# Kernel optimization log

Measured on AMD Instinct MI355X. Metric: run time of the kernel, lower is better.

The kernel has to match this reference:

```python
import jax, jax.numpy as jnp
import numpy as np

N_NODES = 50000
N_EDGES = 800000
N_FEAT = 512
N_HEADS = 8
OUT_PER_HEAD = 32  # nhid // nheads = 256 // 8
ALPHA = 0.2  # LeakyReLU negative slope


def setup_inputs() -> dict:
    key = jax.random.key(0)
    ks = jax.random.split(key, 7)
    h = jax.random.normal(ks[0], (N_NODES, N_FEAT), dtype=jnp.float32)
    src = jax.random.randint(ks[1], (N_EDGES,), 0, N_NODES)
    dst = jax.random.randint(ks[2], (N_EDGES,), 0, N_NODES)
    # per-head linear W: [H, F, O], bias [H, O]; attention vector a: [H, 2O], bias [H]
    W = jax.random.normal(ks[3], (N_HEADS, N_FEAT, OUT_PER_HEAD), dtype=jnp.float32) * 0.05
    Wb = jax.random.normal(ks[4], (N_HEADS, OUT_PER_HEAD), dtype=jnp.float32) * 0.05
    a = jax.random.normal(ks[5], (N_HEADS, 2 * OUT_PER_HEAD), dtype=jnp.float32) * 0.05
    ab = jax.random.normal(ks[6], (N_HEADS,), dtype=jnp.float32) * 0.05
    return {"h": h, "src": src, "dst": dst, "W": W, "Wb": Wb, "a": a, "ab": ab}


def reference(h, src, dst, W, Wb, a, ab):
    N = h.shape[0]
    H, F_in, O = W.shape
    # Per-head projection Wh = W(h): [N, H, O]
    Wh = jnp.einsum('nf,hfo->nho', h, W) + Wb
    # a @ concat(Wh_src, Wh_dst) == a_src @ Wh_src + a_dst @ Wh_dst
    a_src, a_dst = a[:, :O], a[:, O:]
    e_s = jnp.einsum('nho,ho->nh', Wh, a_src)  # [N, H]
    e_d = jnp.einsum('nho,ho->nh', Wh, a_dst)
    e = e_s[src] + e_d[dst] + ab               # [E, H]
    e = jnp.where(e > 0, e, ALPHA * e)         # LeakyReLU
    # Segment softmax over incoming edges of each destination node
    m = jax.ops.segment_max(e, dst, num_segments=N)        # [N, H]
    m = jnp.where(jnp.isfinite(m), m, jnp.zeros_like(m))   # isolated nodes
    w = jnp.exp(e - m[dst])                                # [E, H]
    denom = jax.ops.segment_sum(w, dst, num_segments=N)    # [N, H]
    att = w / jnp.where(denom[dst] > 0, denom[dst], 1.0)   # [E, H]
    # Weighted aggregation of source projections, per head, then concat heads
    out = jax.ops.segment_sum(att[:, :, None] * Wh[src], dst, num_segments=N)  # [N, H, O]
    return out.reshape(N, H * O)
```

## Files before the change

### kernel.cpp

```cpp
#include <hip/hip_runtime.h>
#include <math.h>

#define ALPHA 0.2f

constexpr int F_IN  = 512;
constexpr int HO    = 256;
constexpr int NHEAD = 8;

using bf16x8 = __attribute__((ext_vector_type(8))) short;
using bf16x4 = __attribute__((ext_vector_type(4))) short;
using f32x4  = __attribute__((ext_vector_type(4))) float;

__device__ __forceinline__ ushort f2bf(float f) {
    uint u = __float_as_uint(f);
    uint r = (u + 0x7FFFu + ((u >> 16) & 1u)) >> 16;
    return (ushort)r;
}
__device__ __forceinline__ float bf2f(ushort b) {
    return __uint_as_float(((uint)b) << 16);
}

__global__ __launch_bounds__(256) void prep_kernel(const float* __restrict__ W,
                                                   ushort* __restrict__ Wf,
                                                   const int* __restrict__ dst,
                                                   int* __restrict__ cnt,
                                                   int* __restrict__ rnk, int E) {
    const int bid = blockIdx.x;
    const int t = threadIdx.x;
    if (bid < 64) {
        int g = bid * 256 + t;
        int l   = g & 63;
        int oct = (g >> 6) & 15;
        int ks  = g >> 10;
        int oc  = oct * 16 + (l & 15);
        int hh  = oc >> 5, oo = oc & 31;
        int kb  = ks * 32 + (l >> 4) * 8;
        ushort v[8];
#pragma unroll
        for (int j = 0; j < 8; ++j)
            v[j] = f2bf(W[((size_t)hh * F_IN + kb + j) * 32 + oo]);
        bf16x8 o = { (short)v[0], (short)v[1], (short)v[2], (short)v[3],
                     (short)v[4], (short)v[5], (short)v[6], (short)v[7] };
        *(bf16x8*)(Wf + (size_t)g * 8) = o;
    } else {
        int base = (bid - 64) * 1024;
#pragma unroll
        for (int q = 0; q < 4; ++q) {
            int i = base + q * 256 + t;
            if (i < E) rnk[i] = atomicAdd(&cnt[dst[i]], 1);
        }
    }
}

__global__ __launch_bounds__(256) void scan1_kernel(const int* __restrict__ cnt,
                                                    int* __restrict__ bsum, int N) {
    __shared__ int red[256];
    const int t = threadIdx.x;
    const int b0 = blockIdx.x * 1024;
    int s = 0;
#pragma unroll
    for (int q = 0; q < 4; ++q) {
        int i = b0 + t * 4 + q;
        if (i < N) s += cnt[i];
    }
    red[t] = s;
    __syncthreads();
    for (int st = 128; st > 0; st >>= 1) {
        if (t < st) red[t] += red[t + st];
        __syncthreads();
    }
    if (t == 0) bsum[blockIdx.x] = red[0];
}

__global__ __launch_bounds__(64) void scan2_kernel(int* __restrict__ bsum, int nblk) {
    int l = threadIdx.x;
    int x = (l < nblk) ? bsum[l] : 0;
    int inc = x;
    for (int d = 1; d < 64; d <<= 1) {
        int v = __shfl_up(inc, d);
        if (l >= d) inc += v;
    }
    if (l < nblk) bsum[l] = inc - x;
}

__global__ __launch_bounds__(256) void scan3_kernel(const int* __restrict__ cnt,
                                                    const int* __restrict__ bsum,
                                                    int* __restrict__ off, int N, int E) {
    __shared__ int part[256];
    const int t = threadIdx.x;
    const int b0 = blockIdx.x * 1024;
    int v[4];
    int s = 0;
#pragma unroll
    for (int q = 0; q < 4; ++q) {
        int i = b0 + t * 4 + q;
        v[q] = (i < N) ? cnt[i] : 0;
        s += v[q];
    }
    part[t] = s;
    __syncthreads();
    for (int d = 1; d < 256; d <<= 1) {
        int x = (t >= d) ? part[t - d] : 0;
        __syncthreads();
        part[t] += x;
        __syncthreads();
    }
    int run = bsum[blockIdx.x] + ((t == 0) ? 0 : part[t - 1]);
#pragma unroll
    for (int q = 0; q < 4; ++q) {
        int i = b0 + t * 4 + q;
        if (i < N) { off[i] = run; run += v[q]; }
    }
    if (blockIdx.x == 0 && t == 0) off[N] = E;
}

__global__ __launch_bounds__(256) void place_kernel(const int* __restrict__ src,
                                                    const int* __restrict__ dst,
                                                    const int* __restrict__ rnk,
                                                    const int* __restrict__ off,
                                                    int* __restrict__ se, int E) {
    int base = blockIdx.x * 1024;
#pragma unroll
    for (int q = 0; q < 4; ++q) {
        int i = base + q * 256 + threadIdx.x;
        if (i < E) se[off[dst[i]] + rnk[i]] = src[i];
    }
}

__global__ __launch_bounds__(256, 2) void gemm_kernel(
    const float* __restrict__ h, const ushort* __restrict__ Wf,
    const float* __restrict__ Wb, const float* __restrict__ a,
    ushort* __restrict__ Wh, float* __restrict__ es, float* __restrict__ ed, int N)
{
    __shared__ ushort hs[2][128 * 40];
    const int t = threadIdx.x;
    const int l = t & 63;
    const int w = t >> 6;
    const int l15 = l & 15, l4 = l >> 4;
    const int n0 = blockIdx.x * 128;

    const int sr = t >> 1;
    const int sc = (t & 1) * 16;
    int srow = n0 + sr; if (srow >= N) srow = N - 1;
    const float* hrow = h + (size_t)srow * F_IN + sc;

    f32x4 acc[4][8];
#pragma unroll
    for (int i = 0; i < 4; ++i)
#pragma unroll
        for (int nt = 0; nt < 8; ++nt) acc[i][nt] = (f32x4){0.f, 0.f, 0.f, 0.f};

    {
        float4 v0 = *(const float4*)(hrow);
        float4 v1 = *(const float4*)(hrow + 4);
        float4 v2 = *(const float4*)(hrow + 8);
        float4 v3 = *(const float4*)(hrow + 12);
        bf16x8 o0 = { (short)f2bf(v0.x), (short)f2bf(v0.y), (short)f2bf(v0.z), (short)f2bf(v0.w),
                      (short)f2bf(v1.x), (short)f2bf(v1.y), (short)f2bf(v1.z), (short)f2bf(v1.w) };
        bf16x8 o1 = { (short)f2bf(v2.x), (short)f2bf(v2.y), (short)f2bf(v2.z), (short)f2bf(v2.w),
                      (short)f2bf(v3.x), (short)f2bf(v3.y), (short)f2bf(v3.z), (short)f2bf(v3.w) };
        *(bf16x8*)&hs[0][sr * 40 + sc]     = o0;
        *(bf16x8*)&hs[0][sr * 40 + sc + 8] = o1;
    }
    __syncthreads();

    for (int ks = 0; ks < 16; ++ks) {
        const int cb = ks & 1;
        float4 nx0, nx1, nx2, nx3;
        if (ks < 15) {
            const float* p = hrow + (ks + 1) * 32;
            nx0 = *(const float4*)(p);
            nx1 = *(const float4*)(p + 4);
            nx2 = *(const float4*)(p + 8);
            nx3 = *(const float4*)(p + 12);
        }
        bf16x8 af[4];
#pragma unroll
        for (int i = 0; i < 4; ++i)
            af[i] = *(const bf16x8*)(Wf + ((size_t)((ks * 16 + 4 * w + i) * 64 + l)) * 8);
#pragma unroll
        for (int half = 0; half < 2; ++half) {
            bf16x8 b4[4];
#pragma unroll
            for (int j = 0; j < 4; ++j)
                b4[j] = *(const bf16x8*)&hs[cb][((half * 4 + j) * 16 + l15) * 40 + l4 * 8];
#pragma unroll
            for (int i = 0; i < 4; ++i)
#pragma unroll
                for (int j = 0; j < 4; ++j)
                    acc[i][half * 4 + j] = __builtin_amdgcn_mfma_f32_16x16x32_bf16(
                        af[i], b4[j], acc[i][half * 4 + j], 0, 0, 0);
        }
        if (ks < 15) {
            bf16x8 o0 = { (short)f2bf(nx0.x), (short)f2bf(nx0.y), (short)f2bf(nx0.z), (short)f2bf(nx0.w),
                          (short)f2bf(nx1.x), (short)f2bf(nx1.y), (short)f2bf(nx1.z), (short)f2bf(nx1.w) };
            bf16x8 o1 = { (short)f2bf(nx2.x), (short)f2bf(nx2.y), (short)f2bf(nx2.z), (short)f2bf(nx2.w),
                          (short)f2bf(nx3.x), (short)f2bf(nx3.y), (short)f2bf(nx3.z), (short)f2bf(nx3.w) };
            *(bf16x8*)&hs[cb ^ 1][sr * 40 + sc]     = o0;
            *(bf16x8*)&hs[cb ^ 1][sr * 40 + sc + 8] = o1;
            __syncthreads();
        }
    }

    float4 wb4[4], as4[4], ad4[4];
    int ocb[4];
#pragma unroll
    for (int i = 0; i < 4; ++i) {
        int oc_base = (4 * w + i) * 16 + (l4 << 2);
        ocb[i] = oc_base;
        int head = oc_base >> 5;
        wb4[i] = *(const float4*)(Wb + oc_base);
        as4[i] = *(const float4*)(a + head * 64 + (oc_base & 31));
        ad4[i] = *(const float4*)(a + head * 64 + 32 + (oc_base & 31));
    }
#pragma unroll
    for (int nt = 0; nt < 8; ++nt) {
        int node = n0 + nt * 16 + l15;
        bool ok = node < N;
        float pe[4] = {0.f, 0.f, 0.f, 0.f};
#pragma unroll
        for (int i = 0; i < 4; ++i) {
            f32x4 v = acc[i][nt];
            float r0 = v.x + wb4[i].x, r1 = v.y + wb4[i].y;
            float r2 = v.z + wb4[i].z, r3 = v.w + wb4[i].w;
            if (ok) {
                int head = ocb[i] >> 5, oo = ocb[i] & 31;
                bf16x4 o = { (short)f2bf(r0), (short)f2bf(r1), (short)f2bf(r2), (short)f2bf(r3) };
                *(bf16x4*)(Wh + ((size_t)head * N + node) * 32 + oo) = o;
            }
            float dsv = r0 * as4[i].x + r1 * as4[i].y + r2 * as4[i].z + r3 * as4[i].w;
            float ddv = r0 * ad4[i].x + r1 * ad4[i].y + r2 * ad4[i].z + r3 * ad4[i].w;
            int hp = i >> 1;
            pe[hp] += dsv; pe[2 + hp] += ddv;
        }
#pragma unroll
        for (int q = 0; q < 4; ++q) {
            pe[q] += __shfl_xor(pe[q], 16);
            pe[q] += __shfl_xor(pe[q], 32);
        }
        if (l4 == 0 && ok) {
            es[(size_t)(2 * w)     * N + node] = pe[0];
            es[(size_t)(2 * w + 1) * N + node] = pe[1];
            ed[(size_t)(2 * w)     * N + node] = pe[2];
            ed[(size_t)(2 * w + 1) * N + node] = pe[3];
        }
    }
}

__global__ __launch_bounds__(256) void node_kernel(
    const int* __restrict__ se, const int* __restrict__ off,
    const float* __restrict__ es, const float* __restrict__ ed,
    const float* __restrict__ ab, const ushort* __restrict__ Wh,
    float* __restrict__ out, int N)
{
    const int bid  = blockIdx.x;
    const int hg   = bid & 7;
    const int tile = bid >> 3;
    const int t    = threadIdx.x;
    const int g    = t >> 2;
    const int sub  = t & 3;
    const int n    = tile * 64 + g;
    if (n >= N) return;

    const ushort* WhH = Wh + (size_t)hg * N * 32 + sub * 8;
    const float*  esH = es + (size_t)hg * N;

    const int beg = off[n];
    const int deg = off[n + 1] - beg;
    const float base = ed[(size_t)hg * N + n] + ab[hg];

    float acc[8] = {0.f, 0.f, 0.f, 0.f, 0.f, 0.f, 0.f, 0.f};
    float dsum = 0.f;

    int j = 0;
    for (; j + 1 < deg; j += 2) {
        int s0 = se[beg + j];
        int s1 = se[beg + j + 1];
        float ev0 = esH[s0] + base;
        float ev1 = esH[s1] + base;
        bf16x8 r0 = *(const bf16x8*)(WhH + (size_t)s0 * 32);
        bf16x8 r1 = *(const bf16x8*)(WhH + (size_t)s1 * 32);
        ev0 = ev0 > 0.f ? ev0 : ALPHA * ev0;
        ev1 = ev1 > 0.f ? ev1 : ALPHA * ev1;
        float w0 = __expf(ev0);
        float w1 = __expf(ev1);
#pragma unroll
        for (int i = 0; i < 8; ++i) acc[i] += w0 * bf2f((ushort)r0[i]);
#pragma unroll
        for (int i = 0; i < 8; ++i) acc[i] += w1 * bf2f((ushort)r1[i]);
        dsum += w0 + w1;
    }
    if (j < deg) {
        int s0 = se[beg + j];
        float ev0 = esH[s0] + base;
        bf16x8 r0 = *(const bf16x8*)(WhH + (size_t)s0 * 32);
        ev0 = ev0 > 0.f ? ev0 : ALPHA * ev0;
        float w0 = __expf(ev0);
#pragma unroll
        for (int i = 0; i < 8; ++i) acc[i] += w0 * bf2f((ushort)r0[i]);
        dsum += w0;
    }

    float inv = dsum > 0.f ? 1.f / dsum : 1.f;
    float* op = out + (size_t)n * HO + hg * 32 + sub * 8;
    *(float4*)(op)     = make_float4(acc[0] * inv, acc[1] * inv, acc[2] * inv, acc[3] * inv);
    *(float4*)(op + 4) = make_float4(acc[4] * inv, acc[5] * inv, acc[6] * inv, acc[7] * inv);
}

extern "C" void kernel_launch(void* const* d_in, const int* in_sizes, int n_in,
                              void* d_out, int out_size, void* d_ws, size_t ws_size,
                              hipStream_t stream) {
    const float* h   = (const float*)d_in[0];
    const int*   src = (const int*)  d_in[1];
    const int*   dst = (const int*)  d_in[2];
    const float* W   = (const float*)d_in[3];
    const float* Wb  = (const float*)d_in[4];
    const float* a   = (const float*)d_in[5];
    const float* ab  = (const float*)d_in[6];
    float* out = (float*)d_out;

    const int N = in_sizes[0] / F_IN;
    const int E = in_sizes[1];

    auto align_up = [](size_t x) { return (x + 255) & ~size_t(255); };
    char* p = (char*)d_ws;
    ushort* Wh = (ushort*)p; p += align_up((size_t)N * HO * 2);
    float*  es = (float*)p;  p += align_up((size_t)N * NHEAD * 4);
    float*  ed = (float*)p;  p += align_up((size_t)N * NHEAD * 4);
    int* cnt   = (int*)p;    p += align_up((size_t)N * 4);
    int* off   = (int*)p;    p += align_up((size_t)(N + 1) * 4);
    int* rnk   = (int*)p;    p += align_up((size_t)E * 4);
    int* se    = (int*)p;    p += align_up((size_t)E * 4);
    int* bsum  = (int*)p;    p += align_up((size_t)64 * 4);
    ushort* Wf = (ushort*)p; p += align_up((size_t)16 * 16 * 64 * 8 * 2);

    const int nblk = (N + 1023) / 1024;
    const int EB   = (E + 1023) / 1024;
    const int GB   = (N + 127) / 128;
    const int NT   = (N + 63) / 64;

    hipMemsetAsync(cnt, 0, (size_t)N * sizeof(int), stream);
    prep_kernel<<<64 + EB, 256, 0, stream>>>(W, Wf, dst, cnt, rnk, E);
    scan1_kernel<<<nblk, 256, 0, stream>>>(cnt, bsum, N);
    scan2_kernel<<<1, 64, 0, stream>>>(bsum, nblk);
    scan3_kernel<<<nblk, 256, 0, stream>>>(cnt, bsum, off, N, E);
    place_kernel<<<EB, 256, 0, stream>>>(src, dst, rnk, off, se, E);
    gemm_kernel<<<GB, 256, 0, stream>>>(h, Wf, Wb, a, Wh, es, ed, N);
    node_kernel<<<NT * 8, 256, 0, stream>>>(se, off, es, ed, ab, Wh, out, N);
}
```

Measured before the change: 175.0 us.

## Sort nodes by degree and parallelize edge weight computation across sub-lanes

Builds a degree histogram and a permutation that groups nodes by in-degree (capped at 63), so each wavefront in the node kernel handles nodes of similar degree and suffers less load imbalance. The node kernel now splits the first 32 edges of each node across its 4 sub-lanes: each lane loads its share of source indices and computes their exp weights, then the indices and weights are broadcast with shuffles so that 4 feature rows are gathered per step. Nodes with more than 32 edges fall back to a serial loop for the rest. The cost is extra atomics in the scan kernels, a scattered perm write, and output rows written in permuted order, which is less coalesced.

```diff
diff --git a/kernel.cpp b/kernel.cpp
--- a/kernel.cpp
+++ b/kernel.cpp
@@ -53,7 +53,8 @@
 }
 
 __global__ __launch_bounds__(256) void scan1_kernel(const int* __restrict__ cnt,
-                                                    int* __restrict__ bsum, int N) {
+                                                    int* __restrict__ bsum,
+                                                    int* __restrict__ dhist, int N) {
     __shared__ int red[256];
     const int t = threadIdx.x;
     const int b0 = blockIdx.x * 1024;
@@ -61,7 +62,11 @@
 #pragma unroll
     for (int q = 0; q < 4; ++q) {
         int i = b0 + t * 4 + q;
-        if (i < N) s += cnt[i];
+        if (i < N) {
+            int v = cnt[i];
+            s += v;
+            atomicAdd(&dhist[v > 63 ? 63 : v], 1);
+        }
     }
     red[t] = s;
     __syncthreads();
@@ -72,20 +77,35 @@
     if (t == 0) bsum[blockIdx.x] = red[0];
 }
 
-__global__ __launch_bounds__(64) void scan2_kernel(int* __restrict__ bsum, int nblk) {
-    int l = threadIdx.x;
-    int x = (l < nblk) ? bsum[l] : 0;
-    int inc = x;
-    for (int d = 1; d < 64; d <<= 1) {
-        int v = __shfl_up(inc, d);
-        if (l >= d) inc += v;
-    }
-    if (l < nblk) bsum[l] = inc - x;
+__global__ __launch_bounds__(128) void scan2_kernel(int* __restrict__ bsum, int nblk,
+                                                    const int* __restrict__ dhist,
+                                                    int* __restrict__ dcur) {
+    int t = threadIdx.x;
+    int l = t & 63;
+    if (t < 64) {
+        int x = (l < nblk) ? bsum[l] : 0;
+        int inc = x;
+        for (int d = 1; d < 64; d <<= 1) {
+            int v = __shfl_up(inc, d);
+            if (l >= d) inc += v;
+        }
+        if (l < nblk) bsum[l] = inc - x;
+    } else {
+        int x = dhist[l];
+        int inc = x;
+        for (int d = 1; d < 64; d <<= 1) {
+            int v = __shfl_up(inc, d);
+            if (l >= d) inc += v;
+        }
+        dcur[l] = inc - x;
+    }
 }
 
 __global__ __launch_bounds__(256) void scan3_kernel(const int* __restrict__ cnt,
                                                     const int* __restrict__ bsum,
-                                                    int* __restrict__ off, int N, int E) {
+                                                    int* __restrict__ off,
+                                                    int* __restrict__ dcur,
+                                                    int* __restrict__ perm, int N, int E) {
     __shared__ int part[256];
     const int t = threadIdx.x;
     const int b0 = blockIdx.x * 1024;
@@ -109,7 +129,12 @@
 #pragma unroll
     for (int q = 0; q < 4; ++q) {
         int i = b0 + t * 4 + q;
-        if (i < N) { off[i] = run; run += v[q]; }
+        if (i < N) {
+            off[i] = run; run += v[q];
+            int b = v[q] > 63 ? 63 : v[q];
+            int pos = atomicAdd(&dcur[b], 1);
+            perm[pos] = i;
+        }
     }
     if (blockIdx.x == 0 && t == 0) off[N] = E;
 }
@@ -249,6 +274,7 @@
 
 __global__ __launch_bounds__(256) void node_kernel(
     const int* __restrict__ se, const int* __restrict__ off,
+    const int* __restrict__ perm,
     const float* __restrict__ es, const float* __restrict__ ed,
     const float* __restrict__ ab, const ushort* __restrict__ Wh,
     float* __restrict__ out, int N)
@@ -259,46 +285,76 @@
     const int t    = threadIdx.x;
     const int g    = t >> 2;
     const int sub  = t & 3;
-    const int n    = tile * 64 + g;
-    if (n >= N) return;
-
-    const ushort* WhH = Wh + (size_t)hg * N * 32 + sub * 8;
+    const int gi   = tile * 64 + g;
+    if (gi >= N) return;
+    const int n = perm[gi];
+
+    const ushort* WhH = Wh + (size_t)hg * N * 32;
     const float*  esH = es + (size_t)hg * N;
 
     const int beg = off[n];
     const int deg = off[n + 1] - beg;
     const float base = ed[(size_t)hg * N + n] + ab[hg];
+    const int mdeg = deg < 32 ? deg : 32;
+    const int lbase = (t & 63) & ~3;
+
+    int   sv[8];
+    float wv[8];
+#pragma unroll
+    for (int q = 0; q < 8; ++q) {
+        int idx = sub + 4 * q;
+        sv[q] = (idx < mdeg) ? se[beg + idx] : 0;
+    }
+#pragma unroll
+    for (int q = 0; q < 8; ++q) {
+        int idx = sub + 4 * q;
+        float e = esH[sv[q]] + base;
+        e = e > 0.f ? e : ALPHA * e;
+        wv[q] = (idx < mdeg) ? __expf(e) : 0.f;
+    }
+    float dsum = 0.f;
+#pragma unroll
+    for (int q = 0; q < 8; ++q) dsum += wv[q];
+    dsum += __shfl_xor(dsum, 1);
+    dsum += __shfl_xor(dsum, 2);
 
     float acc[8] = {0.f, 0.f, 0.f, 0.f, 0.f, 0.f, 0.f, 0.f};
-    float dsum = 0.f;
-
-    int j = 0;
-    for (; j + 1 < deg; j += 2) {
-        int s0 = se[beg + j];
-        int s1 = se[beg + j + 1];
-        float ev0 = esH[s0] + base;
-        float ev1 = esH[s1] + base;
-        bf16x8 r0 = *(const bf16x8*)(WhH + (size_t)s0 * 32);
-        bf16x8 r1 = *(const bf16x8*)(WhH + (size_t)s1 * 32);
-        ev0 = ev0 > 0.f ? ev0 : ALPHA * ev0;
-        ev1 = ev1 > 0.f ? ev1 : ALPHA * ev1;
-        float w0 = __expf(ev0);
-        float w1 = __expf(ev1);
+#pragma unroll
+    for (int q = 0; q < 8; ++q) {
+        if (4 * q >= mdeg) break;
+        int   s0 = __shfl(sv[q], lbase + 0);
+        int   s1 = __shfl(sv[q], lbase + 1);
+        int   s2 = __shfl(sv[q], lbase + 2);
+        int   s3 = __shfl(sv[q], lbase + 3);
+        float w0 = __shfl(wv[q], lbase + 0);
+        float w1 = __shfl(wv[q], lbase + 1);
+        float w2 = __shfl(wv[q], lbase + 2);
+        float w3 = __shfl(wv[q], lbase + 3);
+        bf16x8 r0 = *(const bf16x8*)(WhH + (size_t)s0 * 32 + sub * 8);
+        bf16x8 r1 = *(const bf16x8*)(WhH + (size_t)s1 * 32 + sub * 8);
+        bf16x8 r2 = *(const bf16x8*)(WhH + (size_t)s2 * 32 + sub * 8);
+        bf16x8 r3 = *(const bf16x8*)(WhH + (size_t)s3 * 32 + sub * 8);
 #pragma unroll
         for (int i = 0; i < 8; ++i) acc[i] += w0 * bf2f((ushort)r0[i]);
 #pragma unroll
         for (int i = 0; i < 8; ++i) acc[i] += w1 * bf2f((ushort)r1[i]);
-        dsum += w0 + w1;
-    }
-    if (j < deg) {
-        int s0 = se[beg + j];
-        float ev0 = esH[s0] + base;
-        bf16x8 r0 = *(const bf16x8*)(WhH + (size_t)s0 * 32);
-        ev0 = ev0 > 0.f ? ev0 : ALPHA * ev0;
-        float w0 = __expf(ev0);
-#pragma unroll
-        for (int i = 0; i < 8; ++i) acc[i] += w0 * bf2f((ushort)r0[i]);
-        dsum += w0;
+#pragma unroll
+        for (int i = 0; i < 8; ++i) acc[i] += w2 * bf2f((ushort)r2[i]);
+#pragma unroll
+        for (int i = 0; i < 8; ++i) acc[i] += w3 * bf2f((ushort)r3[i]);
+    }
+
+    if (deg > 32) {
+        for (int j = 32; j < deg; ++j) {
+            int s = se[beg + j];
+            float e = esH[s] + base;
+            e = e > 0.f ? e : ALPHA * e;
+            float w = __expf(e);
+            dsum += w;
+            bf16x8 r = *(const bf16x8*)(WhH + (size_t)s * 32 + sub * 8);
+#pragma unroll
+            for (int i = 0; i < 8; ++i) acc[i] += w * bf2f((ushort)r[i]);
+        }
     }
 
     float inv = dsum > 0.f ? 1.f / dsum : 1.f;
@@ -331,7 +387,10 @@
     int* off   = (int*)p;    p += align_up((size_t)(N + 1) * 4);
     int* rnk   = (int*)p;    p += align_up((size_t)E * 4);
     int* se    = (int*)p;    p += align_up((size_t)E * 4);
+    int* perm  = (int*)p;    p += align_up((size_t)N * 4);
     int* bsum  = (int*)p;    p += align_up((size_t)64 * 4);
+    int* dhist = (int*)p;    p += align_up((size_t)64 * 4);
+    int* dcur  = (int*)p;    p += align_up((size_t)64 * 4);
     ushort* Wf = (ushort*)p; p += align_up((size_t)16 * 16 * 64 * 8 * 2);
 
     const int nblk = (N + 1023) / 1024;
@@ -340,11 +399,12 @@
     const int NT   = (N + 63) / 64;
 
     hipMemsetAsync(cnt, 0, (size_t)N * sizeof(int), stream);
+    hipMemsetAsync(dhist, 0, 64 * sizeof(int), stream);
     prep_kernel<<<64 + EB, 256, 0, stream>>>(W, Wf, dst, cnt, rnk, E);
-    scan1_kernel<<<nblk, 256, 0, stream>>>(cnt, bsum, N);
-    scan2_kernel<<<1, 64, 0, stream>>>(bsum, nblk);
-    scan3_kernel<<<nblk, 256, 0, stream>>>(cnt, bsum, off, N, E);
+    scan1_kernel<<<nblk, 256, 0, stream>>>(cnt, bsum, dhist, N);
+    scan2_kernel<<<1, 128, 0, stream>>>(bsum, nblk, dhist, dcur);
+    scan3_kernel<<<nblk, 256, 0, stream>>>(cnt, bsum, off, dcur, perm, N, E);
     place_kernel<<<EB, 256, 0, stream>>>(src, dst, rnk, off, se, E);
     gemm_kernel<<<GB, 256, 0, stream>>>(h, Wf, Wb, a, Wh, es, ed, N);
-    node_kernel<<<NT * 8, 256, 0, stream>>>(se, off, es, ed, ab, Wh, out, N);
-}
+    node_kernel<<<NT * 8, 256, 0, stream>>>(se, off, perm, es, ed, ab, Wh, out, N);
+}
```

Measured after the change: 433.8 us. 2.48x slower.
